# Kernel tuning notes

Measured on AMD Instinct MI355X. Metric: run time of the kernel, lower is better.

## Reference

```python
import jax, jax.numpy as jnp
import numpy as np

MODEL_DIM = 1024
TOTAL_DIM = 1024
N_HEADS = 16
HEAD_DIM = TOTAL_DIM // N_HEADS


def setup_inputs() -> dict:
    key = jax.random.key(0)
    k1, k2, k3 = jax.random.split(key, 3)
    query = jax.random.normal(k1, (2, 2048, MODEL_DIM), dtype=jnp.float32)
    # nn.Linear(model_dim, 3*total_dim, bias=False): store as [in, out] for x @ W
    W_in = jax.random.normal(k2, (MODEL_DIM, 3 * TOTAL_DIM), dtype=jnp.float32) / np.sqrt(MODEL_DIM)
    W_out = jax.random.normal(k3, (TOTAL_DIM, MODEL_DIM), dtype=jnp.float32) / np.sqrt(TOTAL_DIM)
    return {"query": query, "W_in": W_in, "W_out": W_out}


def reference(query, W_in, W_out):
    B, S, _ = query.shape
    qkv = query @ W_in                      # [B, S, 3*D]
    q, k, v = jnp.split(qkv, 3, axis=-1)    # each [B, S, D]

    def to_heads(t):
        return t.reshape(B, S, N_HEADS, HEAD_DIM).transpose(0, 2, 1, 3)  # [B,H,S,d]

    q, k, v = to_heads(q), to_heads(k), to_heads(v)
    scale = 1.0 / np.sqrt(HEAD_DIM).astype(np.float32)
    scores = jnp.einsum('bhqd,bhkd->bhqk', q, k) * scale  # [B,H,S,S]
    causal = jnp.tril(jnp.ones((S, S), dtype=bool))
    scores = jnp.where(causal, scores, jnp.finfo(scores.dtype).min)
    probs = jax.nn.softmax(scores, axis=-1)
    attn = jnp.einsum('bhqk,bhkd->bhqd', probs, v)        # [B,H,S,d]
    attn = attn.transpose(0, 2, 1, 3).reshape(B, S, TOTAL_DIM)
    return attn @ W_out                     # [B, S, model_dim]
```

## Files before the change

### kernel.cpp

```cpp
#include <hip/hip_runtime.h>


typedef __bf16 bf16x8 __attribute__((ext_vector_type(8)));
typedef float f32x4 __attribute__((ext_vector_type(4)));

#define B_   2
#define S_   2048
#define DM   1024
#define NH   16
#define HD   64
#define N3   3072
#define M_   4096

#define SCALE_LOG2E 0.180336884f

__device__ __forceinline__ unsigned short f2bf(float f) {
  unsigned int u = __float_as_uint(f);
  u += 0x7fffu + ((u >> 16) & 1u);
  return (unsigned short)(u >> 16);
}

__device__ __forceinline__ void gload_lds16(void* lds, const void* g) {
  __builtin_amdgcn_global_load_lds(
      (__attribute__((address_space(1))) void*)g,
      (__attribute__((address_space(3))) void*)lds, 16, 0, 0);
}

__global__ __launch_bounds__(256) void f32_to_bf16_vec(
    const float4* __restrict__ in, unsigned short* __restrict__ out, int n4) {
  int i = blockIdx.x * 256 + threadIdx.x;
  if (i < n4) {
    float4 v = in[i];
    ushort4 o;
    o.x = f2bf(v.x); o.y = f2bf(v.y); o.z = f2bf(v.z); o.w = f2bf(v.w);
    *(ushort4*)(&out[(size_t)i * 4]) = o;
  }
}

__global__ __launch_bounds__(256) void transpose_f32_bf16(
    const float* __restrict__ in, unsigned short* __restrict__ out, int R, int C) {
  __shared__ float tile[32][33];
  const int tx = threadIdx.x, ty = threadIdx.y;
  const int x = blockIdx.x * 32 + tx;
  const int y0 = blockIdx.y * 32;
#pragma unroll
  for (int j = 0; j < 32; j += 8)
    tile[ty + j][tx] = in[(size_t)(y0 + ty + j) * C + x];
  __syncthreads();
  const int ox = y0 + tx;
  const int oy0 = blockIdx.x * 32;
#pragma unroll
  for (int j = 0; j < 32; j += 8)
    out[(size_t)(oy0 + ty + j) * R + ox] = f2bf(tile[tx][ty + j]);
}

__global__ __launch_bounds__(256) void transpose_v(
    const unsigned short* __restrict__ qkv, unsigned short* __restrict__ vT) {
  __shared__ unsigned short tile[32][33];
  const int tx = threadIdx.x, ty = threadIdx.y;
  const int c0 = blockIdx.x * 32;
  const int r0 = blockIdx.y * 32;
#pragma unroll
  for (int j = 0; j < 32; j += 8)
    tile[ty + j][tx] = qkv[(size_t)(r0 + ty + j) * N3 + 2 * DM + c0 + tx];
  __syncthreads();
  const int b = r0 >> 11;
  const int srow = (r0 & 2047);
  const int head = c0 >> 6;
#pragma unroll
  for (int j = 0; j < 32; j += 8) {
    const int d = (c0 & 63) + ty + j;
    vT[(size_t)((b * NH + head) * HD + d) * S_ + srow + tx] = tile[tx][ty + j];
  }
}

template <int OUT_BF16>
__global__ __launch_bounds__(256) void gemm_abt(
    const unsigned short* __restrict__ A, const unsigned short* __restrict__ Bt,
    void* __restrict__ Cv, int M, int N, int K) {
  __shared__ __align__(16) unsigned short a_sm[128 * 32];
  __shared__ __align__(16) unsigned short b_sm[128 * 32];
  const int tid = threadIdx.x;
  const int lane = tid & 63, wave = tid >> 6;
  const int quad = lane >> 4, l15 = lane & 15;
  const int row0 = blockIdx.y * 128, col0 = blockIdx.x * 128;
  const int wm = (wave >> 1) * 64, wn = (wave & 1) * 64;

  f32x4 acc[4][4];
#pragma unroll
  for (int i = 0; i < 4; i++)
#pragma unroll
    for (int j = 0; j < 4; j++) acc[i][j] = (f32x4){0.f, 0.f, 0.f, 0.f};

  const int e0 = tid * 8;

  for (int k0 = 0; k0 < K; k0 += 32) {
    __syncthreads();
#pragma unroll
    for (int i = 0; i < 2; i++) {
      int e = e0 + i * 2048;
      int r = e >> 5, c = e & 31;
      gload_lds16(&a_sm[e], &A[(size_t)(row0 + r) * K + k0 + c]);
      gload_lds16(&b_sm[e], &Bt[(size_t)(col0 + r) * K + k0 + c]);
    }
    __syncthreads();

    bf16x8 af[4], bfb[4];
#pragma unroll
    for (int i = 0; i < 4; i++) {
      af[i]  = *(const bf16x8*)&a_sm[(wm + i * 16 + l15) * 32 + quad * 8];
      bfb[i] = *(const bf16x8*)&b_sm[(wn + i * 16 + l15) * 32 + quad * 8];
    }
#pragma unroll
    for (int i = 0; i < 4; i++)
#pragma unroll
      for (int j = 0; j < 4; j++)
        acc[i][j] = __builtin_amdgcn_mfma_f32_16x16x32_bf16(af[i], bfb[j], acc[i][j], 0, 0, 0);
  }

#pragma unroll
  for (int i = 0; i < 4; i++) {
#pragma unroll
    for (int j = 0; j < 4; j++) {
#pragma unroll
      for (int r = 0; r < 4; r++) {
        const int row = row0 + wm + i * 16 + quad * 4 + r;
        const int col = col0 + wn + j * 16 + l15;
        const float v = acc[i][j][r];
        if (OUT_BF16)
          ((unsigned short*)Cv)[(size_t)row * N + col] = f2bf(v);
        else
          ((float*)Cv)[(size_t)row * N + col] = v;
      }
    }
  }
}

__global__ __launch_bounds__(256) void attn_fused2(
    const unsigned short* __restrict__ qkv,
    const unsigned short* __restrict__ vT,
    unsigned short* __restrict__ attnout) {
  const int h = blockIdx.y, b = blockIdx.z;
  const int qt = (b == 0) ? blockIdx.x : (15 - blockIdx.x);
  const int tid = threadIdx.x;
  const int lane = tid & 63, wave = tid >> 6;
  const int quad = lane >> 4, l15 = lane & 15;
  const int sw = l15 & 7;

  __shared__ __align__(16) unsigned short k_sm[64 * 64];
  __shared__ __align__(16) unsigned short vt_sm[64 * 64];
  __shared__ __align__(16) unsigned short p_sm[4 * 32 * 64];

  const int Q0 = qt * 128;

  bf16x8 qf[2][2];
#pragma unroll
  for (int i = 0; i < 2; i++) {
    const int row = b * S_ + Q0 + wave * 32 + i * 16 + l15;
    const unsigned short* qp = qkv + (size_t)row * N3 + h * HD + quad * 8;
    qf[i][0] = *(const bf16x8*)(qp);
    qf[i][1] = *(const bf16x8*)(qp + 32);
  }

  f32x4 o[2][4];
  f32x4 lsum[2];
#pragma unroll
  for (int i = 0; i < 2; i++) {
    lsum[i] = (f32x4){0.f, 0.f, 0.f, 0.f};
#pragma unroll
    for (int n = 0; n < 4; n++) o[i][n] = (f32x4){0.f, 0.f, 0.f, 0.f};
  }

  const int r0s = tid >> 3;
  const int gch = ((tid & 7) ^ (r0s & 7)) * 8;
  const unsigned short* kbase = qkv + (size_t)(b * S_) * N3 + DM + h * HD;
  const unsigned short* vbase = vT + (size_t)((b * NH + h) * HD) * S_;

  const int nt = 2 * qt + 2;
  for (int t = 0; t < nt; t++) {
    __syncthreads();
    {
      const unsigned short* kg = kbase + (size_t)(t * 64) * N3;
      const unsigned short* vg = vbase + t * 64;
      gload_lds16(&k_sm[tid * 8],         kg + (size_t)r0s * N3 + gch);
      gload_lds16(&k_sm[tid * 8 + 2048],  kg + (size_t)(r0s + 32) * N3 + gch);
      gload_lds16(&vt_sm[tid * 8],        vg + (size_t)r0s * S_ + gch);
      gload_lds16(&vt_sm[tid * 8 + 2048], vg + (size_t)(r0s + 32) * S_ + gch);
    }
    __syncthreads();

    f32x4 s[2][4];
#pragma unroll
    for (int n = 0; n < 4; n++) { s[0][n] = (f32x4){0.f,0.f,0.f,0.f}; s[1][n] = (f32x4){0.f,0.f,0.f,0.f}; }
#pragma unroll
    for (int n = 0; n < 4; n++) {
      const int krow = (n * 16 + l15) * 64;
      bf16x8 kf0 = *(const bf16x8*)&k_sm[krow + ((quad ^ sw) << 3)];
      bf16x8 kf1 = *(const bf16x8*)&k_sm[krow + (((4 + quad) ^ sw) << 3)];
      s[0][n] = __builtin_amdgcn_mfma_f32_16x16x32_bf16(qf[0][0], kf0, s[0][n], 0, 0, 0);
      s[0][n] = __builtin_amdgcn_mfma_f32_16x16x32_bf16(qf[0][1], kf1, s[0][n], 0, 0, 0);
      s[1][n] = __builtin_amdgcn_mfma_f32_16x16x32_bf16(qf[1][0], kf0, s[1][n], 0, 0, 0);
      s[1][n] = __builtin_amdgcn_mfma_f32_16x16x32_bf16(qf[1][1], kf1, s[1][n], 0, 0, 0);
    }

    if (t >= 2 * qt) {
#pragma unroll
      for (int i = 0; i < 2; i++)
#pragma unroll
        for (int n = 0; n < 4; n++)
#pragma unroll
          for (int r = 0; r < 4; r++) {
            const int key = t * 64 + n * 16 + l15;
            const int row = Q0 + wave * 32 + i * 16 + quad * 4 + r;
            s[i][n][r] = (key <= row) ? exp2f(s[i][n][r] * SCALE_LOG2E) : 0.f;
          }
    } else {
#pragma unroll
      for (int i = 0; i < 2; i++)
#pragma unroll
        for (int n = 0; n < 4; n++)
#pragma unroll
          for (int r = 0; r < 4; r++)
            s[i][n][r] = exp2f(s[i][n][r] * SCALE_LOG2E);
    }
#pragma unroll
    for (int i = 0; i < 2; i++)
#pragma unroll
      for (int n = 0; n < 4; n++) lsum[i] += s[i][n];

    unsigned short* pw = p_sm + wave * 2048;
#pragma unroll
    for (int i = 0; i < 2; i++)
#pragma unroll
      for (int n = 0; n < 4; n++) {
        const int ch = n * 2 + (l15 >> 3);
        const int within = l15 & 7;
#pragma unroll
        for (int r = 0; r < 4; r++) {
          const int row = i * 16 + quad * 4 + r;
          pw[row * 64 + ((ch ^ (row & 7)) << 3) + within] = f2bf(s[i][n][r]);
        }
      }

#pragma unroll
    for (int c = 0; c < 2; c++) {
      const int chs = ((c * 4 + quad) ^ sw) << 3;
      bf16x8 pf0 = *(const bf16x8*)&pw[l15 * 64 + chs];
      bf16x8 pf1 = *(const bf16x8*)&pw[(16 + l15) * 64 + chs];
#pragma unroll
      for (int n2 = 0; n2 < 4; n2++) {
        bf16x8 vf = *(const bf16x8*)&vt_sm[(n2 * 16 + l15) * 64 + chs];
        o[0][n2] = __builtin_amdgcn_mfma_f32_16x16x32_bf16(pf0, vf, o[0][n2], 0, 0, 0);
        o[1][n2] = __builtin_amdgcn_mfma_f32_16x16x32_bf16(pf1, vf, o[1][n2], 0, 0, 0);
      }
    }
  }

#pragma unroll
  for (int i = 0; i < 2; i++) {
#pragma unroll
    for (int r = 0; r < 4; r++) {
      float l = lsum[i][r];
      l += __shfl_xor(l, 1);
      l += __shfl_xor(l, 2);
      l += __shfl_xor(l, 4);
      l += __shfl_xor(l, 8);
      const float inv = 1.0f / l;
      const int row = b * S_ + Q0 + wave * 32 + i * 16 + quad * 4 + r;
#pragma unroll
      for (int n2 = 0; n2 < 4; n2++)
        attnout[(size_t)row * DM + h * HD + n2 * 16 + l15] = f2bf(o[i][n2][r] * inv);
    }
  }
}

extern "C" void kernel_launch(void* const* d_in, const int* in_sizes, int n_in,
                              void* d_out, int out_size, void* d_ws, size_t ws_size,
                              hipStream_t stream) {
  const float* query = (const float*)d_in[0];
  const float* w_in  = (const float*)d_in[1];
  const float* w_out = (const float*)d_in[2];
  float* out = (float*)d_out;

  char* ws = (char*)d_ws;
  unsigned short* qbf     = (unsigned short*)(ws);
  unsigned short* vT      = (unsigned short*)(ws);
  unsigned short* w_in_t  = (unsigned short*)(ws + 8388608);
  unsigned short* w_out_t = (unsigned short*)(ws + 14680064);
  unsigned short* qkv     = (unsigned short*)(ws + 16777216);
  unsigned short* attn    = (unsigned short*)(ws + 41943040);

  f32_to_bf16_vec<<<dim3(M_ * DM / 1024), dim3(256), 0, stream>>>(
      (const float4*)query, qbf, M_ * DM / 4);
  transpose_f32_bf16<<<dim3(N3 / 32, DM / 32), dim3(32, 8), 0, stream>>>(w_in, w_in_t, DM, N3);
  transpose_f32_bf16<<<dim3(DM / 32, DM / 32), dim3(32, 8), 0, stream>>>(w_out, w_out_t, DM, DM);
  gemm_abt<1><<<dim3(N3 / 128, M_ / 128), dim3(256), 0, stream>>>(qbf, w_in_t, qkv, M_, N3, DM);
  transpose_v<<<dim3(DM / 32, M_ / 32), dim3(32, 8), 0, stream>>>(qkv, vT);
  attn_fused2<<<dim3(S_ / 128, NH, B_), dim3(256), 0, stream>>>(qkv, vT, attn);
  gemm_abt<0><<<dim3(DM / 128, M_ / 128), dim3(256), 0, stream>>>(attn, w_out_t, out, M_, DM, DM);
}
```

Baseline: 213.3 us.

## Restructure attention kernel: 8 waves, double-buffered K/V, register-resident P via bpermute

The attention kernel now runs 512 threads with each wave owning 16 query rows instead of 32. K and V tiles are double-buffered in LDS so the next tile's load is issued while the current one is processed, which removes one barrier per iteration. The MFMA operands are swapped so the score tile comes out transposed; P is then packed to bf16 and redistributed with ds_bpermute instead of being written to and read back from LDS. Waves whose rows lie entirely above the causal diagonal skip the tile, and output stores are vectorized. In exchange the kernel adds more permute instructions, uses a rounding shortcut that is not round-to-nearest-even, and the changed occupancy may not pay off.

```diff
diff --git a/kernel.cpp b/kernel.cpp
--- a/kernel.cpp
+++ b/kernel.cpp
@@ -3,6 +3,7 @@
 
 typedef __bf16 bf16x8 __attribute__((ext_vector_type(8)));
 typedef float f32x4 __attribute__((ext_vector_type(4)));
+typedef int i32x4 __attribute__((ext_vector_type(4)));
 
 #define B_   2
 #define S_   2048
@@ -136,7 +137,7 @@
   }
 }
 
-__global__ __launch_bounds__(256) void attn_fused2(
+__global__ __launch_bounds__(512, 4) void attn_fused3(
     const unsigned short* __restrict__ qkv,
     const unsigned short* __restrict__ vT,
     unsigned short* __restrict__ attnout) {
@@ -147,130 +148,132 @@
   const int quad = lane >> 4, l15 = lane & 15;
   const int sw = l15 & 7;
 
-  __shared__ __align__(16) unsigned short k_sm[64 * 64];
-  __shared__ __align__(16) unsigned short vt_sm[64 * 64];
-  __shared__ __align__(16) unsigned short p_sm[4 * 32 * 64];
+  __shared__ __align__(16) unsigned short k_sm[2 * 4096];
+  __shared__ __align__(16) unsigned short vt_sm[2 * 4096];
 
   const int Q0 = qt * 128;
-
-  bf16x8 qf[2][2];
-#pragma unroll
-  for (int i = 0; i < 2; i++) {
-    const int row = b * S_ + Q0 + wave * 32 + i * 16 + l15;
-    const unsigned short* qp = qkv + (size_t)row * N3 + h * HD + quad * 8;
-    qf[i][0] = *(const bf16x8*)(qp);
-    qf[i][1] = *(const bf16x8*)(qp + 32);
-  }
-
-  f32x4 o[2][4];
-  f32x4 lsum[2];
-#pragma unroll
-  for (int i = 0; i < 2; i++) {
-    lsum[i] = (f32x4){0.f, 0.f, 0.f, 0.f};
-#pragma unroll
-    for (int n = 0; n < 4; n++) o[i][n] = (f32x4){0.f, 0.f, 0.f, 0.f};
-  }
+  const int qrow = Q0 + wave * 16 + l15;
+  const int wrow0 = Q0 + wave * 16;
+
+  bf16x8 qf[2];
+  {
+    const unsigned short* qp = qkv + (size_t)(b * S_ + qrow) * N3 + h * HD + quad * 8;
+    qf[0] = *(const bf16x8*)qp;
+    qf[1] = *(const bf16x8*)(qp + 32);
+  }
+
+  f32x4 o[4];
+#pragma unroll
+  for (int n = 0; n < 4; n++) o[n] = (f32x4){0.f, 0.f, 0.f, 0.f};
+  float lsum = 0.f;
 
   const int r0s = tid >> 3;
   const int gch = ((tid & 7) ^ (r0s & 7)) * 8;
-  const unsigned short* kbase = qkv + (size_t)(b * S_) * N3 + DM + h * HD;
-  const unsigned short* vbase = vT + (size_t)((b * NH + h) * HD) * S_;
+  const unsigned short* kgb = qkv + (size_t)(b * S_ + r0s) * N3 + DM + h * HD + gch;
+  const unsigned short* vgb = vT + (size_t)((b * NH + h) * HD + r0s) * S_ + gch;
+
+  const int addrA = (((quad * 2) & 3) * 16 + l15) * 4;
+  const int addrB = (((quad * 2 + 1) & 3) * 16 + l15) * 4;
 
   const int nt = 2 * qt + 2;
+  gload_lds16(&k_sm[tid * 8], kgb);
+  gload_lds16(&vt_sm[tid * 8], vgb);
+
   for (int t = 0; t < nt; t++) {
     __syncthreads();
-    {
-      const unsigned short* kg = kbase + (size_t)(t * 64) * N3;
-      const unsigned short* vg = vbase + t * 64;
-      gload_lds16(&k_sm[tid * 8],         kg + (size_t)r0s * N3 + gch);
-      gload_lds16(&k_sm[tid * 8 + 2048],  kg + (size_t)(r0s + 32) * N3 + gch);
-      gload_lds16(&vt_sm[tid * 8],        vg + (size_t)r0s * S_ + gch);
-      gload_lds16(&vt_sm[tid * 8 + 2048], vg + (size_t)(r0s + 32) * S_ + gch);
-    }
-    __syncthreads();
-
-    f32x4 s[2][4];
-#pragma unroll
-    for (int n = 0; n < 4; n++) { s[0][n] = (f32x4){0.f,0.f,0.f,0.f}; s[1][n] = (f32x4){0.f,0.f,0.f,0.f}; }
-#pragma unroll
-    for (int n = 0; n < 4; n++) {
-      const int krow = (n * 16 + l15) * 64;
-      bf16x8 kf0 = *(const bf16x8*)&k_sm[krow + ((quad ^ sw) << 3)];
-      bf16x8 kf1 = *(const bf16x8*)&k_sm[krow + (((4 + quad) ^ sw) << 3)];
-      s[0][n] = __builtin_amdgcn_mfma_f32_16x16x32_bf16(qf[0][0], kf0, s[0][n], 0, 0, 0);
-      s[0][n] = __builtin_amdgcn_mfma_f32_16x16x32_bf16(qf[0][1], kf1, s[0][n], 0, 0, 0);
-      s[1][n] = __builtin_amdgcn_mfma_f32_16x16x32_bf16(qf[1][0], kf0, s[1][n], 0, 0, 0);
-      s[1][n] = __builtin_amdgcn_mfma_f32_16x16x32_bf16(qf[1][1], kf1, s[1][n], 0, 0, 0);
-    }
-
-    if (t >= 2 * qt) {
-#pragma unroll
-      for (int i = 0; i < 2; i++)
-#pragma unroll
-        for (int n = 0; n < 4; n++)
-#pragma unroll
-          for (int r = 0; r < 4; r++) {
-            const int key = t * 64 + n * 16 + l15;
-            const int row = Q0 + wave * 32 + i * 16 + quad * 4 + r;
-            s[i][n][r] = (key <= row) ? exp2f(s[i][n][r] * SCALE_LOG2E) : 0.f;
-          }
+    if (t + 1 < nt) {
+      const int nb = ((t + 1) & 1) * 4096;
+      gload_lds16(&k_sm[nb + tid * 8], kgb + (size_t)(t + 1) * 64 * N3);
+      gload_lds16(&vt_sm[nb + tid * 8], vgb + (t + 1) * 64);
+    }
+    if (t * 64 > wrow0 + 15) continue;
+
+    const unsigned short* kb = &k_sm[(t & 1) * 4096];
+    const unsigned short* vb = &vt_sm[(t & 1) * 4096];
+
+    f32x4 s[4];
+#pragma unroll
+    for (int mb = 0; mb < 4; mb++) s[mb] = (f32x4){0.f, 0.f, 0.f, 0.f};
+#pragma unroll
+    for (int mb = 0; mb < 4; mb++) {
+      const int ro = (mb * 16 + l15) * 64;
+      bf16x8 kf0 = *(const bf16x8*)&kb[ro + ((quad ^ sw) << 3)];
+      bf16x8 kf1 = *(const bf16x8*)&kb[ro + (((4 + quad) ^ sw) << 3)];
+      s[mb] = __builtin_amdgcn_mfma_f32_16x16x32_bf16(kf0, qf[0], s[mb], 0, 0, 0);
+      s[mb] = __builtin_amdgcn_mfma_f32_16x16x32_bf16(kf1, qf[1], s[mb], 0, 0, 0);
+    }
+
+    if (t * 64 + 63 <= wrow0) {
+#pragma unroll
+      for (int mb = 0; mb < 4; mb++)
+#pragma unroll
+        for (int r = 0; r < 4; r++)
+          s[mb][r] = exp2f(s[mb][r] * SCALE_LOG2E);
     } else {
-#pragma unroll
-      for (int i = 0; i < 2; i++)
-#pragma unroll
-        for (int n = 0; n < 4; n++)
-#pragma unroll
-          for (int r = 0; r < 4; r++)
-            s[i][n][r] = exp2f(s[i][n][r] * SCALE_LOG2E);
-    }
-#pragma unroll
-    for (int i = 0; i < 2; i++)
-#pragma unroll
-      for (int n = 0; n < 4; n++) lsum[i] += s[i][n];
-
-    unsigned short* pw = p_sm + wave * 2048;
-#pragma unroll
-    for (int i = 0; i < 2; i++)
-#pragma unroll
-      for (int n = 0; n < 4; n++) {
-        const int ch = n * 2 + (l15 >> 3);
-        const int within = l15 & 7;
+      const int kb0 = t * 64 + quad * 4;
+#pragma unroll
+      for (int mb = 0; mb < 4; mb++)
 #pragma unroll
         for (int r = 0; r < 4; r++) {
-          const int row = i * 16 + quad * 4 + r;
-          pw[row * 64 + ((ch ^ (row & 7)) << 3) + within] = f2bf(s[i][n][r]);
+          const float e = exp2f(s[mb][r] * SCALE_LOG2E);
+          s[mb][r] = (kb0 + mb * 16 + r <= qrow) ? e : 0.f;
         }
+    }
+#pragma unroll
+    for (int mb = 0; mb < 4; mb++)
+      lsum += (s[mb][0] + s[mb][1]) + (s[mb][2] + s[mb][3]);
+
+    int pk[4][2];
+#pragma unroll
+    for (int mb = 0; mb < 4; mb++) {
+      const unsigned u0 = __float_as_uint(s[mb][0]) + 0x8000u;
+      const unsigned u1 = __float_as_uint(s[mb][1]) + 0x8000u;
+      const unsigned u2 = __float_as_uint(s[mb][2]) + 0x8000u;
+      const unsigned u3 = __float_as_uint(s[mb][3]) + 0x8000u;
+      pk[mb][0] = (int)__builtin_amdgcn_perm(u1, u0, 0x07060302u);
+      pk[mb][1] = (int)__builtin_amdgcn_perm(u3, u2, 0x07060302u);
+    }
+
+    const bool hi = quad >= 2;
+#pragma unroll
+    for (int ks = 0; ks < 2; ks++) {
+      const int m0 = 2 * ks, m1 = m0 + 1;
+      const int f0a = __builtin_amdgcn_ds_bpermute(addrA, pk[m0][0]);
+      const int f0b = __builtin_amdgcn_ds_bpermute(addrA, pk[m1][0]);
+      const int f1a = __builtin_amdgcn_ds_bpermute(addrA, pk[m0][1]);
+      const int f1b = __builtin_amdgcn_ds_bpermute(addrA, pk[m1][1]);
+      const int f2a = __builtin_amdgcn_ds_bpermute(addrB, pk[m0][0]);
+      const int f2b = __builtin_amdgcn_ds_bpermute(addrB, pk[m1][0]);
+      const int f3a = __builtin_amdgcn_ds_bpermute(addrB, pk[m0][1]);
+      const int f3b = __builtin_amdgcn_ds_bpermute(addrB, pk[m1][1]);
+      i32x4 fr;
+      fr.x = hi ? f0b : f0a;
+      fr.y = hi ? f1b : f1a;
+      fr.z = hi ? f2b : f2a;
+      fr.w = hi ? f3b : f3a;
+      const bf16x8 pfrag = __builtin_bit_cast(bf16x8, fr);
+#pragma unroll
+      for (int mb = 0; mb < 4; mb++) {
+        const int ro = (mb * 16 + l15) * 64;
+        bf16x8 vf = *(const bf16x8*)&vb[ro + (((ks * 4 + quad) ^ sw) << 3)];
+        o[mb] = __builtin_amdgcn_mfma_f32_16x16x32_bf16(vf, pfrag, o[mb], 0, 0, 0);
       }
-
-#pragma unroll
-    for (int c = 0; c < 2; c++) {
-      const int chs = ((c * 4 + quad) ^ sw) << 3;
-      bf16x8 pf0 = *(const bf16x8*)&pw[l15 * 64 + chs];
-      bf16x8 pf1 = *(const bf16x8*)&pw[(16 + l15) * 64 + chs];
-#pragma unroll
-      for (int n2 = 0; n2 < 4; n2++) {
-        bf16x8 vf = *(const bf16x8*)&vt_sm[(n2 * 16 + l15) * 64 + chs];
-        o[0][n2] = __builtin_amdgcn_mfma_f32_16x16x32_bf16(pf0, vf, o[0][n2], 0, 0, 0);
-        o[1][n2] = __builtin_amdgcn_mfma_f32_16x16x32_bf16(pf1, vf, o[1][n2], 0, 0, 0);
-      }
-    }
-  }
-
-#pragma unroll
-  for (int i = 0; i < 2; i++) {
-#pragma unroll
-    for (int r = 0; r < 4; r++) {
-      float l = lsum[i][r];
-      l += __shfl_xor(l, 1);
-      l += __shfl_xor(l, 2);
-      l += __shfl_xor(l, 4);
-      l += __shfl_xor(l, 8);
-      const float inv = 1.0f / l;
-      const int row = b * S_ + Q0 + wave * 32 + i * 16 + quad * 4 + r;
-#pragma unroll
-      for (int n2 = 0; n2 < 4; n2++)
-        attnout[(size_t)row * DM + h * HD + n2 * 16 + l15] = f2bf(o[i][n2][r] * inv);
-    }
+    }
+  }
+
+  float l = lsum;
+  l += __shfl_xor(l, 16);
+  l += __shfl_xor(l, 32);
+  const float inv = 1.0f / l;
+  const size_t grow = (size_t)(b * S_ + qrow);
+#pragma unroll
+  for (int mb = 0; mb < 4; mb++) {
+    ushort4 w;
+    w.x = f2bf(o[mb][0] * inv);
+    w.y = f2bf(o[mb][1] * inv);
+    w.z = f2bf(o[mb][2] * inv);
+    w.w = f2bf(o[mb][3] * inv);
+    *(ushort4*)&attnout[grow * DM + h * HD + mb * 16 + quad * 4] = w;
   }
 }
 
@@ -296,6 +299,6 @@
   transpose_f32_bf16<<<dim3(DM / 32, DM / 32), dim3(32, 8), 0, stream>>>(w_out, w_out_t, DM, DM);
   gemm_abt<1><<<dim3(N3 / 128, M_ / 128), dim3(256), 0, stream>>>(qbf, w_in_t, qkv, M_, N3, DM);
   transpose_v<<<dim3(DM / 32, M_ / 32), dim3(32, 8), 0, stream>>>(qkv, vT);
-  attn_fused2<<<dim3(S_ / 128, NH, B_), dim3(256), 0, stream>>>(qkv, vT, attn);
+  attn_fused3<<<dim3(S_ / 128, NH, B_), dim3(512), 0, stream>>>(qkv, vT, attn);
   gemm_abt<0><<<dim3(DM / 128, M_ / 128), dim3(256), 0, stream>>>(attn, w_out_t, out, M_, DM, DM);
 }
```

New measurement: 203.5 us. 4.6% less time.
